# Kernel optimization log

Measured on AMD Instinct MI355X. Metric: run time of the kernel, lower is better.

## Reference

```python
import jax, jax.numpy as jnp
import numpy as np

B, V, C, NQ, H, PTS, FFN = 2, 6, 128, 1200, 8, 4, 256
SHAPES = [(112, 200), (56, 100), (28, 50), (14, 25)]
LVLS = len(SHAPES)
LTOT = sum(h * w for h, w in SHAPES)
STARTS = np.cumsum([0] + [h * w for h, w in SHAPES])[:-1].tolist()


def _ln(x, g, b):
    m = jnp.mean(x, -1, keepdims=True)
    v = jnp.var(x, -1, keepdims=True)
    return (x - m) * jax.lax.rsqrt(v + 1e-5) * g + b


def _mlp(x, w1, b1, w2, b2):
    return jax.nn.relu(x @ w1 + b1) @ w2 + b2


def setup_inputs():
    ks = iter(jax.random.split(jax.random.key(0), 64))
    def rn(*shape):
        return jax.random.normal(next(ks), shape, jnp.float32) * 0.02
    inp = {}
    inp["img_query_feat"] = jax.random.normal(next(ks), (B, C, NQ), jnp.float32)
    inp["normal_img_query_pos"] = jax.random.normal(next(ks), (B, NQ, 2), jnp.float32)
    for i, (h, w) in enumerate(SHAPES):
        inp["img_feat%d" % i] = jax.random.normal(next(ks), (B, V, C, h, w), jnp.float32)
    inp["normal_img_feats_pos_stack"] = jax.random.uniform(next(ks), (1, LTOT, 2), jnp.float32)
    inp["sp_w1"] = rn(2, C); inp["sp_b1"] = rn(C); inp["sp_w2"] = rn(C, C); inp["sp_b2"] = rn(C)
    inp["cp_w1"] = rn(2, C); inp["cp_b1"] = rn(C); inp["cp_w2"] = rn(C, C); inp["cp_b2"] = rn(C)
    inp["sa_wqkv"] = rn(C, 3 * C); inp["sa_bqkv"] = rn(3 * C); inp["sa_wo"] = rn(C, C); inp["sa_bo"] = rn(C)
    inp["ln1_g"] = jnp.ones((C,), jnp.float32); inp["ln1_b"] = jnp.zeros((C,), jnp.float32)
    inp["d_val_w"] = rn(C, C); inp["d_val_b"] = rn(C)
    inp["d_off_w"] = rn(C, H * LVLS * PTS * 2); inp["d_off_b"] = rn(H * LVLS * PTS * 2)
    inp["d_attn_w"] = rn(C, H * LVLS * PTS); inp["d_attn_b"] = rn(H * LVLS * PTS)
    inp["d_out_w"] = rn(C, C); inp["d_out_b"] = rn(C)
    inp["ln2_g"] = jnp.ones((C,), jnp.float32); inp["ln2_b"] = jnp.zeros((C,), jnp.float32)
    inp["ffn_w1"] = rn(C, FFN); inp["ffn_b1"] = rn(FFN); inp["ffn_w2"] = rn(FFN, C); inp["ffn_b2"] = rn(C)
    inp["ln3_g"] = jnp.ones((C,), jnp.float32); inp["ln3_b"] = jnp.zeros((C,), jnp.float32)
    inp["ph_w1"] = rn(C, C); inp["ph_b1"] = rn(C); inp["ph_w2"] = rn(C, 6); inp["ph_b2"] = rn(6)
    inp["img_query_view"] = jax.random.randint(next(ks), (B, NQ), 0, V)
    return inp


def _forward(img_query_view, img_query_feat, normal_img_query_pos, img_feat0, img_feat1, img_feat2, img_feat3, normal_img_feats_pos_stack, sp_w1, sp_b1, sp_w2, sp_b2, cp_w1, cp_b1, cp_w2, cp_b2, sa_wqkv, sa_bqkv, sa_wo, sa_bo, ln1_g, ln1_b, d_val_w, d_val_b, d_off_w, d_off_b, d_attn_w, d_attn_b, d_out_w, d_out_b, ln2_g, ln2_b, ffn_w1, ffn_b1, ffn_w2, ffn_b2, ln3_g, ln3_b, ph_w1, ph_b1, ph_w2, ph_b2):
    # flatten multi-scale feats: [B, V, C, LTOT]
    feats = jnp.concatenate([f.reshape(B, V, C, -1) for f in (img_feat0, img_feat1, img_feat2, img_feat3)], axis=3)
    ref = jax.nn.sigmoid(normal_img_query_pos)  # [B,NQ,2], shared across levels
    qpe = _mlp(normal_img_query_pos, sp_w1, sp_b1, sp_w2, sp_b2)  # [B,NQ,C] self posembed
    kpe = _mlp(normal_img_feats_pos_stack[0], cp_w1, cp_b1, cp_w2, cp_b2)  # [LTOT,C] cross posembed
    # value projection of (key + key_pos_embed), per view
    value = jnp.einsum('bvcl,cd->bvld', feats, d_val_w) + kpe @ d_val_w + d_val_b  # [B,V,LTOT,C]
    value_flat = value.reshape(B, V * LTOT, C)
    x = img_query_feat.transpose(0, 2, 1)  # [B,NQ,C]
    # ragged per-view grouping: queries interact only within their own view
    same_view = img_query_view[:, :, None] == img_query_view[:, None, :]
    counts = jax.vmap(lambda v: jnp.bincount(v, length=V))(img_query_view)  # [B,V]
    valid = jnp.take_along_axis(counts, img_query_view, axis=1) > 1  # views with <=1 query are skipped
    Ch = C // H
    # --- self attention (masked to same view) ---
    qkv = (x + qpe) @ sa_wqkv + sa_bqkv
    q, k, v = jnp.split(qkv, 3, axis=-1)
    q = q.reshape(B, NQ, H, Ch); k = k.reshape(B, NQ, H, Ch); v = v.reshape(B, NQ, H, Ch)
    logits = jnp.einsum('bnhd,bmhd->bhnm', q, k) / float(np.sqrt(Ch))
    logits = jnp.where(same_view[:, None], logits, -1e9)
    attn = jax.nn.softmax(logits, axis=-1)
    sa_out = jnp.einsum('bhnm,bmhd->bnhd', attn, v).reshape(B, NQ, C) @ sa_wo + sa_bo
    x = _ln(x + sa_out, ln1_g, ln1_b)
    # --- multi-scale deformable cross attention, view-routed per query ---
    qc = x + qpe
    off = (qc @ d_off_w + d_off_b).reshape(B, NQ, H, LVLS, PTS, 2)
    aw = jax.nn.softmax((qc @ d_attn_w + d_attn_b).reshape(B, NQ, H, LVLS * PTS), axis=-1).reshape(B, NQ, H, LVLS, PTS)
    normalizer = jnp.array([[w, h] for h, w in SHAPES], jnp.float32)  # (w,h) per level
    loc = ref[:, :, None, None, None, :] + off / normalizer[None, None, None, :, None, :]
    base = (img_query_view * LTOT)[:, :, None, None].astype(jnp.int32)  # route query to its view
    eyeH = jnp.eye(H, dtype=x.dtype)
    out = jnp.zeros((B, NQ, H, Ch), x.dtype)
    for l, (h, w) in enumerate(SHAPES):
        lx = loc[:, :, :, l, :, 0] * w - 0.5  # grid_sample align_corners=False convention
        ly = loc[:, :, :, l, :, 1] * h - 0.5  # [B,NQ,H,PTS]
        x0 = jnp.floor(lx); y0 = jnp.floor(ly)
        fx = lx - x0; fy = ly - y0
        x0i = x0.astype(jnp.int32); y0i = y0.astype(jnp.int32)
        samp = jnp.zeros((B, NQ, H, PTS, Ch), x.dtype)
        for dy in (0, 1):
            for dx in (0, 1):
                xi = x0i + dx; yi = y0i + dy
                wgt = (fx if dx else 1.0 - fx) * (fy if dy else 1.0 - fy)
                ok = (xi >= 0) & (xi < w) & (yi >= 0) & (yi < h)  # zero padding
                idx = base + STARTS[l] + jnp.clip(yi, 0, h - 1) * w + jnp.clip(xi, 0, w - 1)
                g = jnp.take_along_axis(value_flat, idx.reshape(B, -1)[:, :, None], axis=1)
                g = g.reshape(B, NQ, H, PTS, H, Ch)
                g = jnp.einsum('bnhpqc,hq->bnhpc', g, eyeH)  # head h uses its own channel slice
                samp = samp + jnp.where(ok[..., None], wgt[..., None], 0.0) * g
        out = out + jnp.einsum('bnhp,bnhpc->bnhc', aw[:, :, :, l], samp)
    ca_out = out.reshape(B, NQ, C) @ d_out_w + d_out_b
    x = _ln(x + ca_out, ln2_g, ln2_b)
    x = _ln(x + _mlp(x, ffn_w1, ffn_b1, ffn_w2, ffn_b2), ln3_g, ln3_b)
    x = jnp.where(valid[..., None], x, 0.0)  # skipped views stay zero (scatter-back semantics)
    # --- prediction head: center_offset [B,6,NQ] ---
    res = _mlp(x, ph_w1, ph_b1, ph_w2, ph_b2).transpose(0, 2, 1)
    center_raw = res[:, :2] + normal_img_query_pos.transpose(0, 2, 1)
    new_pos = jax.lax.stop_gradient(center_raw).transpose(0, 2, 1)  # supervision2d=True update
    center = jax.nn.sigmoid(center_raw)
    offs = jax.nn.sigmoid(res[:, 2:])
    bw = offs[:, 0] + offs[:, 2]
    bh = offs[:, 1] + offs[:, 3]
    cx = (2.0 * center[:, 0] - offs[:, 0] + offs[:, 2]) * 0.5
    cy = (2.0 * center[:, 1] - offs[:, 1] + offs[:, 3]) * 0.5
    bbox = jax.lax.stop_gradient(jnp.stack([cx, cy, bw, bh], axis=1))
    return (x.transpose(0, 2, 1), new_pos, center, offs, bbox)


def reference(img_query_feat, normal_img_query_pos, img_feat0, img_feat1, img_feat2, img_feat3, normal_img_feats_pos_stack, sp_w1, sp_b1, sp_w2, sp_b2, cp_w1, cp_b1, cp_w2, cp_b2, sa_wqkv, sa_bqkv, sa_wo, sa_bo, ln1_g, ln1_b, d_val_w, d_val_b, d_off_w, d_off_b, d_attn_w, d_attn_b, d_out_w, d_out_b, ln2_g, ln2_b, ffn_w1, ffn_b1, ffn_w2, ffn_b2, ln3_g, ln3_b, ph_w1, ph_b1, ph_w2, ph_b2, img_query_view):
    return _forward(img_query_view, img_query_feat, normal_img_query_pos, img_feat0, img_feat1, img_feat2, img_feat3, normal_img_feats_pos_stack, sp_w1, sp_b1, sp_w2, sp_b2, cp_w1, cp_b1, cp_w2, cp_b2, sa_wqkv, sa_bqkv, sa_wo, sa_bo, ln1_g, ln1_b, d_val_w, d_val_b, d_off_w, d_off_b, d_attn_w, d_attn_b, d_out_w, d_out_b, ln2_g, ln2_b, ffn_w1, ffn_b1, ffn_w2, ffn_b2, ln3_g, ln3_b, ph_w1, ph_b1, ph_w2, ph_b2)
```

## Files before the change

### kernel.cpp

```cpp
#include <hip/hip_runtime.h>
#include <hip/hip_bf16.h>
#include <math.h>

#define DEV __device__ __forceinline__

#define BB 2
#define VV 6
#define CC 128
#define NQ 1200
#define HH 8
#define PTSN 4
#define FFND 256
#define LVLSN 4
#define LTOT 29750
#define NROWS (BB*NQ)

__constant__ int c_W[4] = {200,100,50,25};
__constant__ int c_H[4] = {112,56,28,14};
__constant__ int c_S[4] = {0,22400,28000,29400};

DEV float bflo(unsigned u){ union{unsigned i; float f;}x; x.i = u<<16; return x.f; }
DEV float bfhi(unsigned u){ union{unsigned i; float f;}x; x.i = u&0xffff0000u; return x.f; }
DEV unsigned short f2bf(float f){ union{float f; unsigned i;}x; x.f=f; unsigned i=x.i;
  return (unsigned short)((i + 0x7fffu + ((i>>16)&1u))>>16); }
DEV unsigned addbf2(unsigned a, unsigned b){
  float lo = bflo(a)+bflo(b); float hi = bfhi(a)+bfhi(b);
  return (unsigned)f2bf(lo) | ((unsigned)f2bf(hi)<<16);
}
DEV float sigm(float z){ return 1.f/(1.f+__expf(-z)); }

typedef __attribute__((ext_vector_type(8))) short bf16x8;
typedef __attribute__((ext_vector_type(4))) float f32x4;

__global__ void k_misc(const int* __restrict__ view, int* __restrict__ order,
                       int* __restrict__ counts,
                       const float* __restrict__ vw, unsigned short* __restrict__ wt,
                       const float* __restrict__ cw2, unsigned short* __restrict__ cw2t,
                       const float* __restrict__ iqf, float* __restrict__ x,
                       const float* __restrict__ pos,
                       const float* __restrict__ w1, const float* __restrict__ b1,
                       const float* __restrict__ w2, const float* __restrict__ b2,
                       float* __restrict__ qpe){
  int bid = blockIdx.x;
  int t = threadIdx.x;
  if(bid < BB){
    if(t < 64){
      int b = bid; int lane = t;
      int base0=0,base1=0,base2=0,base3=0,base4=0,base5=0;
      for(int c0=0;c0<NQ;c0+=64){
        int n = c0 + lane;
        int v = (n<NQ) ? view[b*NQ+n] : -1;
        unsigned long long lower = (lane==63)? 0x7fffffffffffffffull : ((1ull<<lane)-1ull);
        #define BUCKET_STEP(VVV, BASE) { \
          unsigned long long mk = __ballot(v==VVV); \
          if(v==VVV){ int r = BASE + __popcll(mk & lower); order[(b*VV+VVV)*NQ + r] = n; } \
          BASE += __popcll(mk); }
        BUCKET_STEP(0, base0) BUCKET_STEP(1, base1) BUCKET_STEP(2, base2)
        BUCKET_STEP(3, base3) BUCKET_STEP(4, base4) BUCKET_STEP(5, base5)
        #undef BUCKET_STEP
      }
      if(lane==0){
        counts[b*VV+0]=base0; counts[b*VV+1]=base1; counts[b*VV+2]=base2;
        counts[b*VV+3]=base3; counts[b*VV+4]=base4; counts[b*VV+5]=base5;
      }
    }
  } else if(bid < BB+16){
    int d0 = (bid-BB)*8;
    __shared__ float s[128][9];
    #pragma unroll
    for(int p=0;p<4;p++){ int i = t + p*256; int c = i>>3, dd = i&7;
      s[c][dd] = vw[c*128 + d0 + dd]; }
    __syncthreads();
    #pragma unroll
    for(int p=0;p<4;p++){ int i = t + p*256; int dd = i>>7, c = i&127;
      wt[(size_t)(d0+dd)*128 + c] = f2bf(s[c][dd]); }
  } else if(bid < BB+32){
    int d0 = (bid-BB-16)*8;
    __shared__ float s[128][9];
    #pragma unroll
    for(int p=0;p<4;p++){ int i = t + p*256; int c = i>>3, dd = i&7;
      s[c][dd] = cw2[c*128 + d0 + dd]; }
    __syncthreads();
    #pragma unroll
    for(int p=0;p<4;p++){ int i = t + p*256; int dd = i>>7, c = i&127;
      cw2t[(size_t)(d0+dd)*128 + c] = f2bf(s[c][dd]); }
  } else if(bid < BB+32+76){
    __shared__ float tile[128][33];
    int idx = bid - (BB+32);
    int b = idx/38; int n0 = (idx%38)*32;
    for(int i=t;i<128*32;i+=256){ int c=i>>5, nn=i&31; int n=n0+nn;
      tile[c][nn] = (n<NQ)? iqf[((size_t)b*CC + c)*NQ + n] : 0.f; }
    __syncthreads();
    for(int i=t;i<32*128;i+=256){ int nn=i>>7, c=i&127;
      int n=n0+nn; if(n<NQ) x[((size_t)b*NQ+n)*128 + c] = tile[c][nn]; }
  } else {
    __shared__ float hid[4][128];
    int row0 = (bid - (BB+32+76))*4;
    int r = t>>7, d = t&127;
    #pragma unroll
    for(int rr=r; rr<4; rr+=2){
      int row = row0 + rr;
      float p0 = pos[row*2+0], p1 = pos[row*2+1];
      hid[rr][d] = fmaxf(p0*w1[d] + p1*w1[128+d] + b1[d], 0.f);
    }
    __syncthreads();
    #pragma unroll
    for(int rr=r; rr<4; rr+=2){
      float acc = b2[d];
      #pragma unroll 4
      for(int c=0;c<128;c++) acc += hid[rr][c]*w2[c*128 + d];
      qpe[(size_t)(row0+rr)*128+d] = acc;
    }
  }
}

__global__ void __launch_bounds__(256) k_kvpe2(
    const float* __restrict__ kpos,
    const float* __restrict__ cw1, const float* __restrict__ cb1,
    const unsigned short* __restrict__ cw2t, const float* __restrict__ cb2,
    const unsigned short* __restrict__ wt, const float* __restrict__ vb,
    unsigned short* __restrict__ kvpe){
  __shared__ unsigned short h_t[64][136];
  __shared__ unsigned short k_t[64][136];
  int t = threadIdx.x;
  int r0 = blockIdx.x*64;
  int lane = t&63, wave = t>>6;
  int fr = lane&15, kg = lane>>4;

  int p = t & 63;
  int d0 = p*2;
  float w1a0 = cw1[d0],     w1a1 = cw1[d0+1];
  float w1b0 = cw1[128+d0], w1b1 = cw1[128+d0+1];
  float b10 = cb1[d0], b11 = cb1[d0+1];
  #pragma unroll 4
  for(int k=0;k<16;k++){
    int r = wave + k*4;
    int row = r0 + r;
    float p0=0.f, p1=0.f;
    if(row < LTOT){ p0 = kpos[row*2]; p1 = kpos[row*2+1]; }
    float h0 = fmaxf(p0*w1a0 + p1*w1b0 + b10, 0.f);
    float h1 = fmaxf(p0*w1a1 + p1*w1b1 + b11, 0.f);
    *reinterpret_cast<unsigned*>(&h_t[r][d0]) = (unsigned)f2bf(h0) | ((unsigned)f2bf(h1)<<16);
  }
  __syncthreads();

  f32x4 acc[4][2];
  #pragma unroll
  for(int i=0;i<4;i++)
    #pragma unroll
    for(int j=0;j<2;j++) acc[i][j] = (f32x4)0.f;
  #pragma unroll
  for(int ck=0; ck<4; ck++){
    int c0 = ck*32;
    bf16x8 bfr[2], af[4];
    #pragma unroll
    for(int j=0;j<2;j++){ int d = wave*32 + j*16 + fr;
      bfr[j] = *reinterpret_cast<const bf16x8*>(cw2t + (size_t)d*128 + c0 + kg*8); }
    #pragma unroll
    for(int i=0;i<4;i++) af[i] = *reinterpret_cast<const bf16x8*>(&h_t[i*16 + fr][c0 + kg*8]);
    #pragma unroll
    for(int i=0;i<4;i++)
      #pragma unroll
      for(int j=0;j<2;j++)
        acc[i][j] = __builtin_amdgcn_mfma_f32_16x16x32_bf16(af[i], bfr[j], acc[i][j], 0, 0, 0);
  }
  #pragma unroll
  for(int i=0;i<4;i++){
    int rbase = i*16 + kg*4;
    #pragma unroll
    for(int j=0;j<2;j++){
      int d = wave*32 + j*16 + fr;
      float bv_ = cb2[d];
      #pragma unroll
      for(int r=0;r<4;r++) k_t[rbase + r][d] = f2bf(acc[i][j][r] + bv_);
    }
  }
  __syncthreads();

  #pragma unroll
  for(int i=0;i<4;i++)
    #pragma unroll
    for(int j=0;j<2;j++) acc[i][j] = (f32x4)0.f;
  #pragma unroll
  for(int ck=0; ck<4; ck++){
    int c0 = ck*32;
    bf16x8 bfr[2], af[4];
    #pragma unroll
    for(int j=0;j<2;j++){ int d = wave*32 + j*16 + fr;
      bfr[j] = *reinterpret_cast<const bf16x8*>(wt + (size_t)d*128 + c0 + kg*8); }
    #pragma unroll
    for(int i=0;i<4;i++) af[i] = *reinterpret_cast<const bf16x8*>(&k_t[i*16 + fr][c0 + kg*8]);
    #pragma unroll
    for(int i=0;i<4;i++)
      #pragma unroll
      for(int j=0;j<2;j++)
        acc[i][j] = __builtin_amdgcn_mfma_f32_16x16x32_bf16(af[i], bfr[j], acc[i][j], 0, 0, 0);
  }
  __syncthreads();
  unsigned short (*c_l)[136] = h_t;
  #pragma unroll
  for(int i=0;i<4;i++){
    int rbase = i*16 + kg*4;
    #pragma unroll
    for(int j=0;j<2;j++){
      int d = wave*32 + j*16 + fr;
      float bv_ = vb[d];
      #pragma unroll
      for(int r=0;r<4;r++) c_l[rbase + r][d] = f2bf(acc[i][j][r] + bv_);
    }
  }
  __syncthreads();
  #pragma unroll
  for(int p4=0;p4<4;p4++){
    int i = t + p4*256;
    int row = i>>4, seg = i&15;
    int glr = r0 + row;
    if(glr < LTOT){
      uint4 cu = *reinterpret_cast<const uint4*>(&c_l[row][seg*8]);
      *reinterpret_cast<uint4*>(kvpe + (size_t)glr*CC + seg*8) = cu;
    }
  }
}

__global__ void __launch_bounds__(256) k_value6(
    const float* __restrict__ f0, const float* __restrict__ f1,
    const float* __restrict__ f2, const float* __restrict__ f3,
    const unsigned short* __restrict__ kvpe, const unsigned short* __restrict__ wt,
    unsigned short* __restrict__ value){
  __shared__ unsigned short a_t[64][136];
  int t = threadIdx.x;
  int bxy = blockIdx.x;
  int bv = bxy % 12;
  int bx = bxy / 12;
  int lvl, tile;
  if(bx < 350){ lvl=0; tile=bx; }
  else if(bx < 438){ lvl=1; tile=bx-350; }
  else if(bx < 460){ lvl=2; tile=bx-438; }
  else { lvl=3; tile=bx-460; }
  const int HW = (lvl==0)?22400:(lvl==1)?5600:(lvl==2)?1400:350;
  const int startL = (lvl==0)?0:(lvl==1)?22400:(lvl==2)?28000:29400;
  const float* feat = (lvl==0)?f0:(lvl==1)?f1:(lvl==2)?f2:f3;
  const float* fbase = feat + (size_t)bv*128*(size_t)HW;
  int l0 = tile*64;

  int lane = t&63, wave = t>>6;
  int fr = lane&15, kg = lane>>4;

  int l_u = t & 63, oct0 = t>>6;
  int gl = l0 + l_u; bool ok = (gl < HW);
  const float* fcol = fbase + (size_t)(oct0*8)*HW + (ok ? gl : 0);

  float v32[4][8];
  #pragma unroll
  for(int q=0;q<4;q++)
    #pragma unroll
    for(int j=0;j<8;j++)
      v32[q][j] = ok ? fcol[(size_t)(q*32+j)*HW] : 0.f;

  #pragma unroll
  for(int q=0;q<4;q++){
    uint4 u;
    u.x = (unsigned)f2bf(v32[q][0]) | ((unsigned)f2bf(v32[q][1])<<16);
    u.y = (unsigned)f2bf(v32[q][2]) | ((unsigned)f2bf(v32[q][3])<<16);
    u.z = (unsigned)f2bf(v32[q][4]) | ((unsigned)f2bf(v32[q][5])<<16);
    u.w = (unsigned)f2bf(v32[q][6]) | ((unsigned)f2bf(v32[q][7])<<16);
    *reinterpret_cast<uint4*>(&a_t[l_u][oct0*8 + q*32]) = u;
  }
  __syncthreads();

  f32x4 acc[4][2];
  #pragma unroll
  for(int i=0;i<4;i++)
    #pragma unroll
    for(int j=0;j<2;j++) acc[i][j] = (f32x4)0.f;

  #pragma unroll
  for(int ck=0; ck<4; ck++){
    int c0 = ck*32;
    bf16x8 bfr[2];
    #pragma unroll
    for(int j=0;j<2;j++){
      int d = wave*32 + j*16 + fr;
      bfr[j] = *reinterpret_cast<const bf16x8*>(wt + (size_t)d*128 + c0 + kg*8);
    }
    bf16x8 af[4];
    #pragma unroll
    for(int i=0;i<4;i++) af[i] = *reinterpret_cast<const bf16x8*>(&a_t[i*16 + fr][c0 + kg*8]);
    #pragma unroll
    for(int i=0;i<4;i++)
      #pragma unroll
      for(int j=0;j<2;j++)
        acc[i][j] = __builtin_amdgcn_mfma_f32_16x16x32_bf16(af[i], bfr[j], acc[i][j], 0, 0, 0);
  }

  __syncthreads();
  unsigned short (*c_l)[136] = a_t;
  #pragma unroll
  for(int i=0;i<4;i++){
    int rbase = i*16 + kg*4;
    #pragma unroll
    for(int j=0;j<2;j++){
      int d = wave*32 + j*16 + fr;
      #pragma unroll
      for(int r=0;r<4;r++) c_l[rbase + r][d] = f2bf(acc[i][j][r]);
    }
  }
  __syncthreads();
  #pragma unroll
  for(int p=0;p<4;p++){
    int i = t + p*256;
    int row = i>>4, seg = i&15;
    int glr = l0 + row;
    if(glr < HW){
      uint4 cu = *reinterpret_cast<const uint4*>(&c_l[row][seg*8]);
      const uint4 ku = *reinterpret_cast<const uint4*>(kvpe + (size_t)(startL+glr)*CC + seg*8);
      uint4 ou;
      ou.x = addbf2(cu.x, ku.x); ou.y = addbf2(cu.y, ku.y);
      ou.z = addbf2(cu.z, ku.z); ou.w = addbf2(cu.w, ku.w);
      *reinterpret_cast<uint4*>(value + ((size_t)bv*LTOT + startL + glr)*CC + seg*8) = ou;
    }
  }
}

template<int K, int N, int R, bool RELU>
__global__ void k_matvec(const float* __restrict__ in, const float* __restrict__ in2,
                         const float* __restrict__ W, const float* __restrict__ bias,
                         float* __restrict__ out, int nrows){
  int r0 = blockIdx.x*R; int d = threadIdx.x;
  __shared__ float s_in[R][K];
  for(int i=d;i<R*K;i+=N){
    int r=i/K, c=i%K; int row=r0+r;
    float v=0.f;
    if(row<nrows){ v = in[(size_t)row*K+c]; if(in2) v += in2[(size_t)row*K+c]; }
    s_in[r][c]=v;
  }
  __syncthreads();
  float acc[R];
  #pragma unroll
  for(int r=0;r<R;r++) acc[r]=bias[d];
  #pragma unroll 4
  for(int c=0;c<K;c++){ float wv = W[(size_t)c*N+d];
    #pragma unroll
    for(int r=0;r<R;r++) acc[r] += s_in[r][c]*wv; }
  #pragma unroll
  for(int r=0;r<R;r++){
    int row=r0+r;
    if(row<nrows){ float v=acc[r]; if(RELU) v=fmaxf(v,0.f); out[(size_t)row*N+d]=v; }
  }
}

#define QT2 64
#define KT2 128
__global__ void __launch_bounds__(256) k_attn_v(const float* __restrict__ qkv,
        const int* __restrict__ order, const int* __restrict__ counts,
        float* __restrict__ att){
  int qt = blockIdx.x;
  int vh = blockIdx.y; int v = vh>>3, h = vh&7;
  int b = blockIdx.z;
  int C = counts[b*VV+v];
  int q0 = qt*QT2;
  if(q0 >= C) return;
  const int* ord = order + (size_t)(b*VV+v)*NQ;
  int t = threadIdx.x;
  __shared__ float q_s[QT2][17];
  __shared__ int qn_s[QT2];
  __shared__ float k_s[KT2][16];
  __shared__ float v_s[KT2][16];
  __shared__ float red[4][QT2][18];
  for(int i=t;i<QT2;i+=256){ int qi=q0+i; qn_s[i] = (qi<C)? ord[qi] : -1; }
  __syncthreads();
  for(int i=t;i<QT2*16;i+=256){ int r=i>>4,c=i&15; int n=qn_s[r];
    q_s[r][c] = (n>=0)? qkv[((size_t)b*NQ+n)*384 + h*16 + c] : 0.f; }
  int qi = t&63, sub = t>>6;
  float m = -1e30f, s = 0.f, acc[16];
  #pragma unroll
  for(int c=0;c<16;c++) acc[c]=0.f;
  for(int k0=0; k0<C; k0+=KT2){
    int kn = C-k0; if(kn>KT2) kn=KT2;
    __syncthreads();
    for(int i=t;i<KT2*16;i+=256){ int r=i>>4,c=i&15;
      float kv=0.f, vv=0.f;
      if(r<kn){ int n=ord[k0+r]; size_t base=((size_t)b*NQ+n)*384 + h*16 + c;
        kv = qkv[base+128]; vv = qkv[base+256]; }
      k_s[r][c]=kv; v_s[r][c]=vv; }
    __syncthreads();
    for(int mm=sub; mm<kn; mm+=4){
      float l=0.f;
      #pragma unroll
      for(int c=0;c<16;c++) l += q_s[qi][c]*k_s[mm][c];
      l *= 0.25f;
      float newm = fmaxf(m,l);
      float e = __expf(l - newm);
      if(newm > m){
        float rr = __expf(m - newm);
        s *= rr;
        #pragma unroll
        for(int c=0;c<16;c++) acc[c]*=rr;
        m = newm;
      }
      s += e;
      #pragma unroll
      for(int c=0;c<16;c++) acc[c] += e*v_s[mm][c];
    }
  }
  red[sub][qi][0]=m; red[sub][qi][1]=s;
  #pragma unroll
  for(int c=0;c<16;c++) red[sub][qi][2+c]=acc[c];
  __syncthreads();
  if(sub==0){
    int n = qn_s[qi];
    if(n>=0){
      float M=-1e30f;
      #pragma unroll
      for(int j=0;j<4;j++) M=fmaxf(M,red[j][qi][0]);
      float S=0.f; float o[16];
      #pragma unroll
      for(int c=0;c<16;c++) o[c]=0.f;
      #pragma unroll
      for(int j=0;j<4;j++){ float e=__expf(red[j][qi][0]-M); S += e*red[j][qi][1];
        #pragma unroll
        for(int c=0;c<16;c++) o[c] += e*red[j][qi][2+c]; }
      float inv = 1.f/S;
      #pragma unroll
      for(int c=0;c<16;c++) att[((size_t)b*NQ+n)*128 + h*16 + c] = o[c]*inv;
    }
  }
}

__global__ void k_proj_ln1(const float* __restrict__ in, const float* __restrict__ W,
                          const float* __restrict__ bias, const float* __restrict__ resid,
                          const float* __restrict__ g, const float* __restrict__ bb,
                          const float* __restrict__ qpe, float* __restrict__ xout,
                          float* __restrict__ qc){
  int r0 = blockIdx.x*8; int d = threadIdx.x;
  __shared__ float s_in[8][128];
  __shared__ float s_m[8][2][2];
  for(int i=d;i<8*128;i+=128){ int r=i>>7, c=i&127; s_in[r][c] = in[(size_t)(r0+r)*128 + c]; }
  __syncthreads();
  float acc[8];
  #pragma unroll
  for(int r=0;r<8;r++) acc[r]=bias[d];
  #pragma unroll 4
  for(int c=0;c<128;c++){ float wv = W[c*128+d];
    #pragma unroll
    for(int r=0;r<8;r++) acc[r] += s_in[r][c]*wv; }
  float v[8];
  int lane = d&63, wid = d>>6;
  #pragma unroll
  for(int r=0;r<8;r++){
    v[r] = acc[r] + resid[(size_t)(r0+r)*128 + d];
    float s1=v[r], s2=v[r]*v[r];
    for(int o=32;o>0;o>>=1){ s1 += __shfl_down(s1,o); s2 += __shfl_down(s2,o); }
    if(lane==0){ s_m[r][wid][0]=s1; s_m[r][wid][1]=s2; }
  }
  __syncthreads();
  #pragma unroll
  for(int r=0;r<8;r++){
    float S1=s_m[r][0][0]+s_m[r][1][0], S2=s_m[r][0][1]+s_m[r][1][1];
    float mean=S1*(1.f/128.f), var=S2*(1.f/128.f)-mean*mean;
    float rs=rsqrtf(var+1e-5f);
    float o=(v[r]-mean)*rs*g[d]+bb[d];
    xout[(size_t)(r0+r)*128+d]=o;
    qc[(size_t)(r0+r)*128+d]=o+qpe[(size_t)(r0+r)*128+d];
  }
}

__global__ void k_off_aw(const float* __restrict__ qc,
                         const float* __restrict__ dow, const float* __restrict__ dob,
                         const float* __restrict__ daw, const float* __restrict__ dab,
                         float* __restrict__ offb, float* __restrict__ awb){
  int r0 = blockIdx.x*8; int t = threadIdx.x;
  __shared__ float s_in[8][128];
  __shared__ float s_aw[8][130];
  for(int i=t;i<8*128;i+=384){ int r=i>>7, c=i&127; s_in[r][c]=qc[(size_t)(r0+r)*128+c]; }
  __syncthreads();
  if(t < 256){
    int d = t;
    float acc[8];
    #pragma unroll
    for(int r=0;r<8;r++) acc[r]=dob[d];
    #pragma unroll 4
    for(int c=0;c<128;c++){ float wv = dow[(size_t)c*256+d];
      #pragma unroll
      for(int r=0;r<8;r++) acc[r] += s_in[r][c]*wv; }
    #pragma unroll
    for(int r=0;r<8;r++) offb[(size_t)(r0+r)*256+d]=acc[r];
  } else {
    int d = t - 256;
    float acc[8];
    #pragma unroll
    for(int r=0;r<8;r++) acc[r]=dab[d];
    #pragma unroll 4
    for(int c=0;c<128;c++){ float wv = daw[(size_t)c*128+d];
      #pragma unroll
      for(int r=0;r<8;r++) acc[r] += s_in[r][c]*wv; }
    #pragma unroll
    for(int r=0;r<8;r++) s_aw[r][d]=acc[r];
  }
  __syncthreads();
  if(t < 64){
    int r = t>>3, h = t&7;
    float mx=-1e30f;
    #pragma unroll
    for(int i=0;i<16;i++) mx = fmaxf(mx, s_aw[r][h*16+i]);
    float e[16]; float sm=0.f;
    #pragma unroll
    for(int i=0;i<16;i++){ e[i]=__expf(s_aw[r][h*16+i]-mx); sm+=e[i]; }
    float inv = 1.f/sm;
    #pragma unroll
    for(int i=0;i<16;i++) awb[(size_t)(r0+r)*128 + h*16+i] = e[i]*inv;
  }
}

__global__ void k_sample(const float* __restrict__ qpos, const int* __restrict__ view,
                         const float* __restrict__ offb, const float* __restrict__ awb,
                         const unsigned short* __restrict__ value, float* __restrict__ ca){
  int n = blockIdx.x, b = blockIdx.y;
  size_t row = (size_t)b*NQ + n;
  int t = threadIdx.x;
  int h = t>>4, lp = t&15, lvl = lp>>2;
  float rx = sigm(qpos[row*2]), ry = sigm(qpos[row*2+1]);
  int vw = view[row];
  int w = c_W[lvl], hh = c_H[lvl];
  float ox = offb[row*256 + t*2], oy = offb[row*256 + t*2+1];
  float a = awb[row*128 + t];
  float lx = rx*(float)w + ox - 0.5f;
  float ly = ry*(float)hh + oy - 0.5f;
  float x0f = floorf(lx), y0f = floorf(ly);
  float fx = lx - x0f, fy = ly - y0f;
  int x0 = (int)x0f, y0 = (int)y0f;
  float samp[16];
  #pragma unroll
  for(int c=0;c<16;c++) samp[c]=0.f;
  size_t brow = ((size_t)(b*VV + vw))*LTOT + c_S[lvl];
  #pragma unroll
  for(int dy=0;dy<2;dy++){
    #pragma unroll
    for(int dx=0;dx<2;dx++){
      int xi=x0+dx, yi=y0+dy;
      if(xi<0||xi>=w||yi<0||yi>=hh) continue;
      float wt = (dx?fx:(1.f-fx))*(dy?fy:(1.f-fy));
      const uint4* vp = reinterpret_cast<const uint4*>(value + (brow + (size_t)yi*w + xi)*CC + h*16);
      uint4 u0 = vp[0], u1 = vp[1];
      samp[0] += wt*bflo(u0.x); samp[1] += wt*bfhi(u0.x);
      samp[2] += wt*bflo(u0.y); samp[3] += wt*bfhi(u0.y);
      samp[4] += wt*bflo(u0.z); samp[5] += wt*bfhi(u0.z);
      samp[6] += wt*bflo(u0.w); samp[7] += wt*bfhi(u0.w);
      samp[8] += wt*bflo(u1.x); samp[9] += wt*bfhi(u1.x);
      samp[10]+= wt*bflo(u1.y); samp[11]+= wt*bfhi(u1.y);
      samp[12]+= wt*bflo(u1.z); samp[13]+= wt*bfhi(u1.z);
      samp[14]+= wt*bflo(u1.w); samp[15]+= wt*bfhi(u1.w);
    }
  }
  __shared__ float sred[128][17];
  #pragma unroll
  for(int c=0;c<16;c++) sred[t][c] = a*samp[c];
  __syncthreads();
  int h2=t>>4, c2=t&15;
  float sum=0.f;
  #pragma unroll
  for(int j=0;j<16;j++) sum += sred[h2*16+j][c2];
  ca[row*128 + t] = sum;
}

__global__ void __launch_bounds__(128) k_tail(
    const float* __restrict__ ca, const float* __restrict__ dOw, const float* __restrict__ dOb,
    const float* __restrict__ xres,
    const float* __restrict__ ln2_g, const float* __restrict__ ln2_b,
    const float* __restrict__ fw1, const float* __restrict__ fb1,
    const float* __restrict__ fw2, const float* __restrict__ fb2,
    const float* __restrict__ ln3_g, const float* __restrict__ ln3_b,
    const float* __restrict__ pw1, const float* __restrict__ pb1,
    const float* __restrict__ pw2, const float* __restrict__ pb2,
    const int* __restrict__ counts, const int* __restrict__ view,
    const float* __restrict__ pos, float* __restrict__ dout){
  int r0 = blockIdx.x*4; int d = threadIdx.x;
  __shared__ float s_a[4][256];
  __shared__ float s_x[4][128];
  __shared__ float s_m[4][2][2];
  __shared__ float s_res[4][6];
  int lane = d&63, wid = d>>6;

  #pragma unroll
  for(int r=0;r<4;r++) s_a[r][d] = ca[(size_t)(r0+r)*128 + d];
  __syncthreads();

  float acc[4];
  #pragma unroll
  for(int r=0;r<4;r++) acc[r]=dOb[d];
  #pragma unroll 4
  for(int c=0;c<128;c++){ float wv = dOw[c*128+d];
    #pragma unroll
    for(int r=0;r<4;r++) acc[r] += s_a[r][c]*wv; }
  float v[4];
  #pragma unroll
  for(int r=0;r<4;r++){
    v[r] = acc[r] + xres[(size_t)(r0+r)*128 + d];
    float s1=v[r], s2=v[r]*v[r];
    for(int o=32;o>0;o>>=1){ s1 += __shfl_down(s1,o); s2 += __shfl_down(s2,o); }
    if(lane==0){ s_m[r][wid][0]=s1; s_m[r][wid][1]=s2; }
  }
  __syncthreads();
  #pragma unroll
  for(int r=0;r<4;r++){
    float S1=s_m[r][0][0]+s_m[r][1][0], S2=s_m[r][0][1]+s_m[r][1][1];
    float mean=S1*(1.f/128.f), var=S2*(1.f/128.f)-mean*mean;
    float rs=rsqrtf(var+1e-5f);
    s_x[r][d]=(v[r]-mean)*rs*ln2_g[d]+ln2_b[d];
  }
  __syncthreads();

  float a2a[4], a2b[4];
  #pragma unroll
  for(int r=0;r<4;r++){ a2a[r]=fb1[d]; a2b[r]=fb1[d+128]; }
  #pragma unroll 4
  for(int c=0;c<128;c++){ float w0 = fw1[c*256+d], w1_ = fw1[c*256+d+128];
    #pragma unroll
    for(int r=0;r<4;r++){ float xv = s_x[r][c]; a2a[r] += xv*w0; a2b[r] += xv*w1_; } }
  __syncthreads();
  #pragma unroll
  for(int r=0;r<4;r++){ s_a[r][d]=fmaxf(a2a[r],0.f); s_a[r][d+128]=fmaxf(a2b[r],0.f); }
  __syncthreads();

  float a3[4];
  #pragma unroll
  for(int r=0;r<4;r++) a3[r]=fb2[d];
  #pragma unroll 4
  for(int c=0;c<256;c++){ float wv = fw2[c*128+d];
    #pragma unroll
    for(int r=0;r<4;r++) a3[r] += s_a[r][c]*wv; }
  #pragma unroll
  for(int r=0;r<4;r++){
    v[r] = a3[r] + s_x[r][d];
    float s1=v[r], s2=v[r]*v[r];
    for(int o=32;o>0;o>>=1){ s1 += __shfl_down(s1,o); s2 += __shfl_down(s2,o); }
    if(lane==0){ s_m[r][wid][0]=s1; s_m[r][wid][1]=s2; }
  }
  __syncthreads();
  #pragma unroll
  for(int r=0;r<4;r++){
    float S1=s_m[r][0][0]+s_m[r][1][0], S2=s_m[r][0][1]+s_m[r][1][1];
    float mean=S1*(1.f/128.f), var=S2*(1.f/128.f)-mean*mean;
    float rs=rsqrtf(var+1e-5f);
    float o=(v[r]-mean)*rs*ln3_g[d]+ln3_b[d];
    int row=r0+r; int b=row/NQ, n=row%NQ;
    bool val = counts[b*VV + view[row]] > 1;
    float oz = val ? o : 0.f;
    s_x[r][d]=oz;
    dout[((size_t)b*CC + d)*NQ + n]=oz;
  }
  __syncthreads();

  float a4[4];
  #pragma unroll
  for(int r=0;r<4;r++) a4[r]=pb1[d];
  #pragma unroll 4
  for(int c=0;c<128;c++){ float wv = pw1[c*128+d];
    #pragma unroll
    for(int r=0;r<4;r++) a4[r] += s_x[r][c]*wv; }
  #pragma unroll
  for(int r=0;r<4;r++) s_a[r][d]=fmaxf(a4[r],0.f);
  __syncthreads();

  if(d < 24){
    int r = d/6, o = d%6;
    float a5 = pb2[o];
    #pragma unroll 4
    for(int c=0;c<128;c++) a5 += s_a[r][c]*pw2[c*6+o];
    s_res[r][o] = a5;
  }
  __syncthreads();
  if(d < 4){
    int r = d; int row = r0+r; int b=row/NQ, n=row%NQ;
    const int O1 = BB*CC*NQ;
    const int O2 = O1 + BB*NQ*2;
    const int O3 = O2 + BB*2*NQ;
    const int O4 = O3 + BB*4*NQ;
    float p0=pos[row*2], p1=pos[row*2+1];
    float cr0 = s_res[r][0]+p0, cr1 = s_res[r][1]+p1;
    dout[O1 + row*2]   = cr0;
    dout[O1 + row*2+1] = cr1;
    float cen0 = sigm(cr0), cen1 = sigm(cr1);
    dout[O2 + (b*2+0)*NQ + n] = cen0;
    dout[O2 + (b*2+1)*NQ + n] = cen1;
    float f0=sigm(s_res[r][2]), f1=sigm(s_res[r][3]), f2=sigm(s_res[r][4]), f3=sigm(s_res[r][5]);
    dout[O3 + (b*4+0)*NQ + n] = f0;
    dout[O3 + (b*4+1)*NQ + n] = f1;
    dout[O3 + (b*4+2)*NQ + n] = f2;
    dout[O3 + (b*4+3)*NQ + n] = f3;
    float bw=f0+f2, bh=f1+f3;
    float cx=(2.f*cen0 - f0 + f2)*0.5f;
    float cy=(2.f*cen1 - f1 + f3)*0.5f;
    dout[O4 + (b*4+0)*NQ + n] = cx;
    dout[O4 + (b*4+1)*NQ + n] = cy;
    dout[O4 + (b*4+2)*NQ + n] = bw;
    dout[O4 + (b*4+3)*NQ + n] = bh;
  }
}

extern "C" void kernel_launch(void* const* d_in, const int* in_sizes, int n_in,
                              void* d_out, int out_size, void* d_ws, size_t ws_size,
                              hipStream_t stream){
  (void)in_sizes; (void)n_in; (void)out_size; (void)ws_size;
  const float* in_iqf  = (const float*)d_in[0];
  const float* in_qpos = (const float*)d_in[1];
  const float* in_feat[4] = {(const float*)d_in[2],(const float*)d_in[3],(const float*)d_in[4],(const float*)d_in[5]};
  const float* in_kpos = (const float*)d_in[6];
  const float* sp_w1=(const float*)d_in[7], *sp_b1=(const float*)d_in[8], *sp_w2=(const float*)d_in[9], *sp_b2=(const float*)d_in[10];
  const float* cp_w1=(const float*)d_in[11], *cp_b1=(const float*)d_in[12], *cp_w2=(const float*)d_in[13], *cp_b2=(const float*)d_in[14];
  const float* sa_wqkv=(const float*)d_in[15], *sa_bqkv=(const float*)d_in[16], *sa_wo=(const float*)d_in[17], *sa_bo=(const float*)d_in[18];
  const float* ln1_g=(const float*)d_in[19], *ln1_b=(const float*)d_in[20];
  const float* dvw=(const float*)d_in[21], *dvb=(const float*)d_in[22];
  const float* dow=(const float*)d_in[23], *dob=(const float*)d_in[24];
  const float* daw=(const float*)d_in[25], *dab=(const float*)d_in[26];
  const float* dOw=(const float*)d_in[27], *dOb=(const float*)d_in[28];
  const float* ln2_g=(const float*)d_in[29], *ln2_b=(const float*)d_in[30];
  const float* fw1=(const float*)d_in[31], *fb1=(const float*)d_in[32], *fw2=(const float*)d_in[33], *fb2=(const float*)d_in[34];
  const float* ln3_g=(const float*)d_in[35], *ln3_b=(const float*)d_in[36];
  const float* pw1=(const float*)d_in[37], *pb1=(const float*)d_in[38], *pw2=(const float*)d_in[39], *pb2=(const float*)d_in[40];
  const int* in_view = (const int*)d_in[41];
  float* out = (float*)d_out;

  char* ws = (char*)d_ws;
  unsigned short* value = (unsigned short*)ws;
  unsigned short* kvpe  = (unsigned short*)(ws + 91392000);
  float* f = (float*)(ws + 91392000 + 7616000);
  float* qpe  = f;
  float* x    = f + 307200;
  float* qkv  = f + 614400;
  float* att  = f + 1536000;
  float* qc   = f + 1843200;
  float* offb = f + 2150400;
  float* awb  = f + 2764800;
  float* ca   = f + 3072000;
  int* counts = (int*)(f + 4300800);
  int* order  = (int*)(f + 4300816);
  unsigned short* wtb   = (unsigned short*)(f + 4315216);
  unsigned short* cw2tb = (unsigned short*)(f + 4323408);

  k_misc<<<dim3(BB+32+76+600),dim3(256),0,stream>>>(in_view,order,counts,dvw,wtb,
      cp_w2,cw2tb,in_iqf,x,in_qpos,sp_w1,sp_b1,sp_w2,sp_b2,qpe);
  k_kvpe2<<<dim3((LTOT+63)/64),dim3(256),0,stream>>>(in_kpos,cp_w1,cp_b1,cw2tb,cp_b2,wtb,dvb,kvpe);
  k_value6<<<dim3(466*12),dim3(256),0,stream>>>(in_feat[0],in_feat[1],in_feat[2],in_feat[3],kvpe,wtb,value);
  k_matvec<128,384,8,false><<<dim3(NROWS/8),dim3(384),0,stream>>>(x,qpe,sa_wqkv,sa_bqkv,qkv,NROWS);
  k_attn_v<<<dim3((NQ+QT2-1)/QT2, VV*HH, BB),dim3(256),0,stream>>>(qkv,order,counts,att);
  k_proj_ln1<<<dim3(NROWS/8),dim3(128),0,stream>>>(att,sa_wo,sa_bo,x,ln1_g,ln1_b,qpe,x,qc);
  k_off_aw<<<dim3(NROWS/8),dim3(384),0,stream>>>(qc,dow,dob,daw,dab,offb,awb);
  k_sample<<<dim3(NQ,BB),dim3(128),0,stream>>>(in_qpos,in_view,offb,awb,value,ca);
  k_tail<<<dim3(NROWS/4),dim3(128),0,stream>>>(ca,dOw,dOb,x,ln2_g,ln2_b,
      fw1,fb1,fw2,fb2,ln3_g,ln3_b,pw1,pb1,pw2,pb2,counts,in_view,in_qpos,out);
}
```

Measured before the change: 238.4 us.

## Retile value projection to 256-position tiles with float4 loads and staged K-chunks

The value projection kernel now processes 256 spatial positions per 512-thread block instead of 64 per 256-thread block. It reads feature maps with coalesced float4 loads, staging fp32 data in LDS per 32-channel chunk and converting to bf16 when building MFMA fragments. Each wave computes a 64x64 output tile, which gives more reuse of the weight fragments, and the epilogue is written in two halves through shared memory. In exchange, each block now syncs more often per chunk, there are fewer blocks, and the strided LDS reads of 8 channel rows may hit bank conflicts.

```diff
diff --git a/kernel.cpp b/kernel.cpp
--- a/kernel.cpp
+++ b/kernel.cpp
@@ -222,102 +222,120 @@
   }
 }
 
-__global__ void __launch_bounds__(256) k_value6(
+__global__ void __launch_bounds__(512) k_value7(
     const float* __restrict__ f0, const float* __restrict__ f1,
     const float* __restrict__ f2, const float* __restrict__ f3,
     const unsigned short* __restrict__ kvpe, const unsigned short* __restrict__ wt,
     unsigned short* __restrict__ value){
-  __shared__ unsigned short a_t[64][136];
+  __shared__ __align__(16) char smem[35840];
+  float (*a_f)[265] = (float(*)[265])smem;
+  unsigned short (*c_l)[136] = (unsigned short(*)[136])smem;
   int t = threadIdx.x;
   int bxy = blockIdx.x;
   int bv = bxy % 12;
   int bx = bxy / 12;
   int lvl, tile;
-  if(bx < 350){ lvl=0; tile=bx; }
-  else if(bx < 438){ lvl=1; tile=bx-350; }
-  else if(bx < 460){ lvl=2; tile=bx-438; }
-  else { lvl=3; tile=bx-460; }
+  if(bx < 88){ lvl=0; tile=bx; }
+  else if(bx < 110){ lvl=1; tile=bx-88; }
+  else if(bx < 116){ lvl=2; tile=bx-110; }
+  else { lvl=3; tile=bx-116; }
   const int HW = (lvl==0)?22400:(lvl==1)?5600:(lvl==2)?1400:350;
   const int startL = (lvl==0)?0:(lvl==1)?22400:(lvl==2)?28000:29400;
   const float* feat = (lvl==0)?f0:(lvl==1)?f1:(lvl==2)?f2:f3;
   const float* fbase = feat + (size_t)bv*128*(size_t)HW;
-  int l0 = tile*64;
+  int l0 = tile*256;
 
   int lane = t&63, wave = t>>6;
+  int lgrp = wave>>1, dgrp = wave&1;
   int fr = lane&15, kg = lane>>4;
 
-  int l_u = t & 63, oct0 = t>>6;
-  int gl = l0 + l_u; bool ok = (gl < HW);
-  const float* fcol = fbase + (size_t)(oct0*8)*HW + (ok ? gl : 0);
-
-  float v32[4][8];
-  #pragma unroll
-  for(int q=0;q<4;q++)
-    #pragma unroll
-    for(int j=0;j<8;j++)
-      v32[q][j] = ok ? fcol[(size_t)(q*32+j)*HW] : 0.f;
-
-  #pragma unroll
-  for(int q=0;q<4;q++){
-    uint4 u;
-    u.x = (unsigned)f2bf(v32[q][0]) | ((unsigned)f2bf(v32[q][1])<<16);
-    u.y = (unsigned)f2bf(v32[q][2]) | ((unsigned)f2bf(v32[q][3])<<16);
-    u.z = (unsigned)f2bf(v32[q][4]) | ((unsigned)f2bf(v32[q][5])<<16);
-    u.w = (unsigned)f2bf(v32[q][6]) | ((unsigned)f2bf(v32[q][7])<<16);
-    *reinterpret_cast<uint4*>(&a_t[l_u][oct0*8 + q*32]) = u;
-  }
-  __syncthreads();
-
-  f32x4 acc[4][2];
+  f32x4 acc[4][4];
   #pragma unroll
   for(int i=0;i<4;i++)
     #pragma unroll
-    for(int j=0;j<2;j++) acc[i][j] = (f32x4)0.f;
-
-  #pragma unroll
+    for(int j=0;j<4;j++) acc[i][j] = (f32x4)0.f;
+
+  int lq = t & 63;
+  int cu_ = t >> 6;
+  int gl4 = l0 + lq*4;
+
   for(int ck=0; ck<4; ck++){
     int c0 = ck*32;
-    bf16x8 bfr[2];
-    #pragma unroll
-    for(int j=0;j<2;j++){
-      int d = wave*32 + j*16 + fr;
+    float4 v[4];
+    #pragma unroll
+    for(int p=0;p<4;p++){
+      int c = cu_ + p*8;
+      const float* src = fbase + (size_t)(c0+c)*HW + gl4;
+      if(gl4 + 4 <= HW){ v[p] = *reinterpret_cast<const float4*>(src); }
+      else {
+        float e0 = (gl4+0<HW)? src[0] : 0.f;
+        float e1 = (gl4+1<HW)? src[1] : 0.f;
+        float e2 = (gl4+2<HW)? src[2] : 0.f;
+        float e3 = (gl4+3<HW)? src[3] : 0.f;
+        v[p] = make_float4(e0,e1,e2,e3);
+      }
+    }
+    __syncthreads();
+    #pragma unroll
+    for(int p=0;p<4;p++){
+      int c = cu_ + p*8;
+      *reinterpret_cast<float4*>(&a_f[c][lq*4]) = v[p];
+    }
+    __syncthreads();
+    bf16x8 bfr[4];
+    #pragma unroll
+    for(int j=0;j<4;j++){
+      int d = dgrp*64 + j*16 + fr;
       bfr[j] = *reinterpret_cast<const bf16x8*>(wt + (size_t)d*128 + c0 + kg*8);
     }
-    bf16x8 af[4];
-    #pragma unroll
-    for(int i=0;i<4;i++) af[i] = *reinterpret_cast<const bf16x8*>(&a_t[i*16 + fr][c0 + kg*8]);
-    #pragma unroll
-    for(int i=0;i<4;i++)
-      #pragma unroll
-      for(int j=0;j<2;j++)
-        acc[i][j] = __builtin_amdgcn_mfma_f32_16x16x32_bf16(af[i], bfr[j], acc[i][j], 0, 0, 0);
-  }
-
-  __syncthreads();
-  unsigned short (*c_l)[136] = a_t;
-  #pragma unroll
-  for(int i=0;i<4;i++){
-    int rbase = i*16 + kg*4;
-    #pragma unroll
-    for(int j=0;j<2;j++){
-      int d = wave*32 + j*16 + fr;
-      #pragma unroll
-      for(int r=0;r<4;r++) c_l[rbase + r][d] = f2bf(acc[i][j][r]);
-    }
-  }
-  __syncthreads();
-  #pragma unroll
-  for(int p=0;p<4;p++){
-    int i = t + p*256;
-    int row = i>>4, seg = i&15;
-    int glr = l0 + row;
-    if(glr < HW){
-      uint4 cu = *reinterpret_cast<const uint4*>(&c_l[row][seg*8]);
-      const uint4 ku = *reinterpret_cast<const uint4*>(kvpe + (size_t)(startL+glr)*CC + seg*8);
-      uint4 ou;
-      ou.x = addbf2(cu.x, ku.x); ou.y = addbf2(cu.y, ku.y);
-      ou.z = addbf2(cu.z, ku.z); ou.w = addbf2(cu.w, ku.w);
-      *reinterpret_cast<uint4*>(value + ((size_t)bv*LTOT + startL + glr)*CC + seg*8) = ou;
+    #pragma unroll
+    for(int i=0;i<4;i++){
+      int l = lgrp*64 + i*16 + fr;
+      float a8[8];
+      #pragma unroll
+      for(int q=0;q<8;q++) a8[q] = a_f[kg*8+q][l];
+      bf16x8 af;
+      unsigned u0 = (unsigned)f2bf(a8[0]) | ((unsigned)f2bf(a8[1])<<16);
+      unsigned u1 = (unsigned)f2bf(a8[2]) | ((unsigned)f2bf(a8[3])<<16);
+      unsigned u2 = (unsigned)f2bf(a8[4]) | ((unsigned)f2bf(a8[5])<<16);
+      unsigned u3 = (unsigned)f2bf(a8[6]) | ((unsigned)f2bf(a8[7])<<16);
+      unsigned* ap = reinterpret_cast<unsigned*>(&af);
+      ap[0]=u0; ap[1]=u1; ap[2]=u2; ap[3]=u3;
+      #pragma unroll
+      for(int j=0;j<4;j++)
+        acc[i][j] = __builtin_amdgcn_mfma_f32_16x16x32_bf16(af, bfr[j], acc[i][j], 0, 0, 0);
+    }
+  }
+
+  #pragma unroll
+  for(int hs=0; hs<2; hs++){
+    __syncthreads();
+    if((lgrp>>1) == hs){
+      #pragma unroll
+      for(int i=0;i<4;i++){
+        int lrow = (lgrp&1)*64 + i*16 + kg*4;
+        #pragma unroll
+        for(int j=0;j<4;j++){
+          int d = dgrp*64 + j*16 + fr;
+          #pragma unroll
+          for(int r=0;r<4;r++) c_l[lrow + r][d] = f2bf(acc[i][j][r]);
+        }
+      }
+    }
+    __syncthreads();
+    #pragma unroll
+    for(int p=0;p<4;p++){
+      int i = t + p*512;
+      int row = i>>4, seg = i&15;
+      int glr = l0 + hs*128 + row;
+      if(glr < HW){
+        uint4 cu2 = *reinterpret_cast<const uint4*>(&c_l[row][seg*8]);
+        const uint4 ku = *reinterpret_cast<const uint4*>(kvpe + (size_t)(startL+glr)*CC + seg*8);
+        uint4 ou;
+        ou.x = addbf2(cu2.x, ku.x); ou.y = addbf2(cu2.y, ku.y);
+        ou.z = addbf2(cu2.z, ku.z); ou.w = addbf2(cu2.w, ku.w);
+        *reinterpret_cast<uint4*>(value + ((size_t)bv*LTOT + startL + glr)*CC + seg*8) = ou;
+      }
     }
   }
 }
@@ -741,7 +759,7 @@
   k_misc<<<dim3(BB+32+76+600),dim3(256),0,stream>>>(in_view,order,counts,dvw,wtb,
       cp_w2,cw2tb,in_iqf,x,in_qpos,sp_w1,sp_b1,sp_w2,sp_b2,qpe);
   k_kvpe2<<<dim3((LTOT+63)/64),dim3(256),0,stream>>>(in_kpos,cp_w1,cp_b1,cw2tb,cp_b2,wtb,dvb,kvpe);
-  k_value6<<<dim3(466*12),dim3(256),0,stream>>>(in_feat[0],in_feat[1],in_feat[2],in_feat[3],kvpe,wtb,value);
+  k_value7<<<dim3(118*12),dim3(512),0,stream>>>(in_feat[0],in_feat[1],in_feat[2],in_feat[3],kvpe,wtb,value);
   k_matvec<128,384,8,false><<<dim3(NROWS/8),dim3(384),0,stream>>>(x,qpe,sa_wqkv,sa_bqkv,qkv,NROWS);
   k_attn_v<<<dim3((NQ+QT2-1)/QT2, VV*HH, BB),dim3(256),0,stream>>>(qkv,order,counts,att);
   k_proj_ln1<<<dim3(NROWS/8),dim3(128),0,stream>>>(att,sa_wo,sa_bo,x,ln1_g,ln1_b,qpe,x,qc);
```

After: 273.2 us. 14.6% more time.

## Merge QKV projection into value kernel and fuse out-proj/LN1 with offset kernel

Applied to the files above, without the earlier changes.

The QKV matvec becomes 300 extra leading blocks of the value-projection kernel, so the two independent workloads share one launch and can overlap. The attention output projection with LayerNorm1 is fused into the offset/attention-weight kernel, keeping the query-plus-position tensor in shared memory instead of writing and re-reading a global qc buffer. This removes two launches and one global round trip. In exchange, the QKV blocks run 256 threads over 384 outputs (a serial second pass for some threads) and the fused kernel leaves most threads idle during the projection phase.

```diff
diff --git a/kernel.cpp b/kernel.cpp
--- a/kernel.cpp
+++ b/kernel.cpp
@@ -222,14 +222,39 @@
   }
 }
 
-__global__ void __launch_bounds__(256) k_value6(
+#define QKVB 300
+__global__ void __launch_bounds__(256) k_value_qkv(
     const float* __restrict__ f0, const float* __restrict__ f1,
     const float* __restrict__ f2, const float* __restrict__ f3,
     const unsigned short* __restrict__ kvpe, const unsigned short* __restrict__ wt,
-    unsigned short* __restrict__ value){
+    unsigned short* __restrict__ value,
+    const float* __restrict__ x, const float* __restrict__ qpe,
+    const float* __restrict__ sa_wqkv, const float* __restrict__ sa_bqkv,
+    float* __restrict__ qkv){
   __shared__ unsigned short a_t[64][136];
+  __shared__ float s_q[8][128];
   int t = threadIdx.x;
-  int bxy = blockIdx.x;
+  int bid = blockIdx.x;
+  if(bid < QKVB){
+    int r0 = bid*8;
+    for(int i=t;i<1024;i+=256){ int r=i>>7, c=i&127;
+      size_t row = (size_t)(r0+r);
+      s_q[r][c] = x[row*128+c] + qpe[row*128+c]; }
+    __syncthreads();
+    for(int d=t; d<384; d+=256){
+      float acc[8];
+      #pragma unroll
+      for(int r=0;r<8;r++) acc[r]=sa_bqkv[d];
+      #pragma unroll 4
+      for(int c=0;c<128;c++){ float wv = sa_wqkv[c*384+d];
+        #pragma unroll
+        for(int r=0;r<8;r++) acc[r] += s_q[r][c]*wv; }
+      #pragma unroll
+      for(int r=0;r<8;r++) qkv[(size_t)(r0+r)*384+d]=acc[r];
+    }
+    return;
+  }
+  int bxy = bid - QKVB;
   int bv = bxy % 12;
   int bx = bxy / 12;
   int lvl, tile;
@@ -319,33 +344,6 @@
       ou.z = addbf2(cu.z, ku.z); ou.w = addbf2(cu.w, ku.w);
       *reinterpret_cast<uint4*>(value + ((size_t)bv*LTOT + startL + glr)*CC + seg*8) = ou;
     }
-  }
-}
-
-template<int K, int N, int R, bool RELU>
-__global__ void k_matvec(const float* __restrict__ in, const float* __restrict__ in2,
-                         const float* __restrict__ W, const float* __restrict__ bias,
-                         float* __restrict__ out, int nrows){
-  int r0 = blockIdx.x*R; int d = threadIdx.x;
-  __shared__ float s_in[R][K];
-  for(int i=d;i<R*K;i+=N){
-    int r=i/K, c=i%K; int row=r0+r;
-    float v=0.f;
-    if(row<nrows){ v = in[(size_t)row*K+c]; if(in2) v += in2[(size_t)row*K+c]; }
-    s_in[r][c]=v;
-  }
-  __syncthreads();
-  float acc[R];
-  #pragma unroll
-  for(int r=0;r<R;r++) acc[r]=bias[d];
-  #pragma unroll 4
-  for(int c=0;c<K;c++){ float wv = W[(size_t)c*N+d];
-    #pragma unroll
-    for(int r=0;r<R;r++) acc[r] += s_in[r][c]*wv; }
-  #pragma unroll
-  for(int r=0;r<R;r++){
-    int row=r0+r;
-    if(row<nrows){ float v=acc[r]; if(RELU) v=fmaxf(v,0.f); out[(size_t)row*N+d]=v; }
   }
 }
 
@@ -427,52 +425,52 @@
   }
 }
 
-__global__ void k_proj_ln1(const float* __restrict__ in, const float* __restrict__ W,
-                          const float* __restrict__ bias, const float* __restrict__ resid,
-                          const float* __restrict__ g, const float* __restrict__ bb,
-                          const float* __restrict__ qpe, float* __restrict__ xout,
-                          float* __restrict__ qc){
-  int r0 = blockIdx.x*8; int d = threadIdx.x;
-  __shared__ float s_in[8][128];
+__global__ void __launch_bounds__(384) k_q2(
+    const float* __restrict__ att, const float* __restrict__ sa_wo, const float* __restrict__ sa_bo,
+    float* __restrict__ x, const float* __restrict__ ln1_g, const float* __restrict__ ln1_b,
+    const float* __restrict__ qpe,
+    const float* __restrict__ dow, const float* __restrict__ dob,
+    const float* __restrict__ daw, const float* __restrict__ dab,
+    float* __restrict__ offb, float* __restrict__ awb){
+  int r0 = blockIdx.x*8; int t = threadIdx.x;
+  __shared__ float s_att[8][128];
+  __shared__ float s_qc[8][128];
   __shared__ float s_m[8][2][2];
-  for(int i=d;i<8*128;i+=128){ int r=i>>7, c=i&127; s_in[r][c] = in[(size_t)(r0+r)*128 + c]; }
-  __syncthreads();
-  float acc[8];
-  #pragma unroll
-  for(int r=0;r<8;r++) acc[r]=bias[d];
-  #pragma unroll 4
-  for(int c=0;c<128;c++){ float wv = W[c*128+d];
-    #pragma unroll
-    for(int r=0;r<8;r++) acc[r] += s_in[r][c]*wv; }
+  __shared__ float s_aw[8][130];
+  for(int i=t;i<1024;i+=384){ int r=i>>7, c=i&127; s_att[r][c]=att[(size_t)(r0+r)*128+c]; }
+  __syncthreads();
+  int lane = t&63, wid = (t>>6)&1;
   float v[8];
-  int lane = d&63, wid = d>>6;
-  #pragma unroll
-  for(int r=0;r<8;r++){
-    v[r] = acc[r] + resid[(size_t)(r0+r)*128 + d];
-    float s1=v[r], s2=v[r]*v[r];
-    for(int o=32;o>0;o>>=1){ s1 += __shfl_down(s1,o); s2 += __shfl_down(s2,o); }
-    if(lane==0){ s_m[r][wid][0]=s1; s_m[r][wid][1]=s2; }
-  }
-  __syncthreads();
-  #pragma unroll
-  for(int r=0;r<8;r++){
-    float S1=s_m[r][0][0]+s_m[r][1][0], S2=s_m[r][0][1]+s_m[r][1][1];
-    float mean=S1*(1.f/128.f), var=S2*(1.f/128.f)-mean*mean;
-    float rs=rsqrtf(var+1e-5f);
-    float o=(v[r]-mean)*rs*g[d]+bb[d];
-    xout[(size_t)(r0+r)*128+d]=o;
-    qc[(size_t)(r0+r)*128+d]=o+qpe[(size_t)(r0+r)*128+d];
-  }
-}
-
-__global__ void k_off_aw(const float* __restrict__ qc,
-                         const float* __restrict__ dow, const float* __restrict__ dob,
-                         const float* __restrict__ daw, const float* __restrict__ dab,
-                         float* __restrict__ offb, float* __restrict__ awb){
-  int r0 = blockIdx.x*8; int t = threadIdx.x;
-  __shared__ float s_in[8][128];
-  __shared__ float s_aw[8][130];
-  for(int i=t;i<8*128;i+=384){ int r=i>>7, c=i&127; s_in[r][c]=qc[(size_t)(r0+r)*128+c]; }
+  if(t < 128){
+    int d = t;
+    float acc[8];
+    #pragma unroll
+    for(int r=0;r<8;r++) acc[r]=sa_bo[d];
+    #pragma unroll 4
+    for(int c=0;c<128;c++){ float wv = sa_wo[c*128+d];
+      #pragma unroll
+      for(int r=0;r<8;r++) acc[r] += s_att[r][c]*wv; }
+    #pragma unroll
+    for(int r=0;r<8;r++){
+      v[r] = acc[r] + x[(size_t)(r0+r)*128 + d];
+      float s1=v[r], s2=v[r]*v[r];
+      for(int o=32;o>0;o>>=1){ s1 += __shfl_down(s1,o); s2 += __shfl_down(s2,o); }
+      if(lane==0){ s_m[r][wid][0]=s1; s_m[r][wid][1]=s2; }
+    }
+  }
+  __syncthreads();
+  if(t < 128){
+    int d = t;
+    #pragma unroll
+    for(int r=0;r<8;r++){
+      float S1=s_m[r][0][0]+s_m[r][1][0], S2=s_m[r][0][1]+s_m[r][1][1];
+      float mean=S1*(1.f/128.f), var=S2*(1.f/128.f)-mean*mean;
+      float rs=rsqrtf(var+1e-5f);
+      float o=(v[r]-mean)*rs*ln1_g[d]+ln1_b[d];
+      x[(size_t)(r0+r)*128+d]=o;
+      s_qc[r][d]=o+qpe[(size_t)(r0+r)*128+d];
+    }
+  }
   __syncthreads();
   if(t < 256){
     int d = t;
@@ -482,7 +480,7 @@
     #pragma unroll 4
     for(int c=0;c<128;c++){ float wv = dow[(size_t)c*256+d];
       #pragma unroll
-      for(int r=0;r<8;r++) acc[r] += s_in[r][c]*wv; }
+      for(int r=0;r<8;r++) acc[r] += s_qc[r][c]*wv; }
     #pragma unroll
     for(int r=0;r<8;r++) offb[(size_t)(r0+r)*256+d]=acc[r];
   } else {
@@ -493,7 +491,7 @@
     #pragma unroll 4
     for(int c=0;c<128;c++){ float wv = daw[(size_t)c*128+d];
       #pragma unroll
-      for(int r=0;r<8;r++) acc[r] += s_in[r][c]*wv; }
+      for(int r=0;r<8;r++) acc[r] += s_qc[r][c]*wv; }
     #pragma unroll
     for(int r=0;r<8;r++) s_aw[r][d]=acc[r];
   }
@@ -729,7 +727,6 @@
   float* x    = f + 307200;
   float* qkv  = f + 614400;
   float* att  = f + 1536000;
-  float* qc   = f + 1843200;
   float* offb = f + 2150400;
   float* awb  = f + 2764800;
   float* ca   = f + 3072000;
@@ -741,11 +738,11 @@
   k_misc<<<dim3(BB+32+76+600),dim3(256),0,stream>>>(in_view,order,counts,dvw,wtb,
       cp_w2,cw2tb,in_iqf,x,in_qpos,sp_w1,sp_b1,sp_w2,sp_b2,qpe);
   k_kvpe2<<<dim3((LTOT+63)/64),dim3(256),0,stream>>>(in_kpos,cp_w1,cp_b1,cw2tb,cp_b2,wtb,dvb,kvpe);
-  k_value6<<<dim3(466*12),dim3(256),0,stream>>>(in_feat[0],in_feat[1],in_feat[2],in_feat[3],kvpe,wtb,value);
-  k_matvec<128,384,8,false><<<dim3(NROWS/8),dim3(384),0,stream>>>(x,qpe,sa_wqkv,sa_bqkv,qkv,NROWS);
+  k_value_qkv<<<dim3(QKVB + 466*12),dim3(256),0,stream>>>(in_feat[0],in_feat[1],in_feat[2],in_feat[3],
+      kvpe,wtb,value,x,qpe,sa_wqkv,sa_bqkv,qkv);
   k_attn_v<<<dim3((NQ+QT2-1)/QT2, VV*HH, BB),dim3(256),0,stream>>>(qkv,order,counts,att);
-  k_proj_ln1<<<dim3(NROWS/8),dim3(128),0,stream>>>(att,sa_wo,sa_bo,x,ln1_g,ln1_b,qpe,x,qc);
-  k_off_aw<<<dim3(NROWS/8),dim3(384),0,stream>>>(qc,dow,dob,daw,dab,offb,awb);
+  k_q2<<<dim3(NROWS/8),dim3(384),0,stream>>>(att,sa_wo,sa_bo,x,ln1_g,ln1_b,qpe,
+      dow,dob,daw,dab,offb,awb);
   k_sample<<<dim3(NQ,BB),dim3(128),0,stream>>>(in_qpos,in_view,offb,awb,value,ca);
   k_tail<<<dim3(NROWS/4),dim3(128),0,stream>>>(ca,dOw,dOb,x,ln2_g,ln2_b,
       fw1,fb1,fw2,fb2,ln3_g,ln3_b,pw1,pb1,pw2,pb2,counts,in_view,in_qpos,out);
```

After: 226.0 us. 1.06x faster.
